# Kernel optimization log

Measured on AMD Instinct MI355X. Metric: run time of the kernel, lower is better.

The kernel has to match this reference:

```python
import jax, jax.numpy as jnp
import numpy as np

S, B, D1, D2 = 256, 128, 1024, 1024
H1 = (D1 + D1) // 2  # 1024
H2 = (D1 + D2) // 2  # 1024


def setup_inputs() -> dict:
    key = jax.random.key(0)
    ks = jax.random.split(key, 11)
    s = lambda k, shp, fan_in: jax.random.normal(k, shp, jnp.float32) * (1.0 / np.sqrt(fan_in))
    return {
        "feature1": jax.random.normal(ks[0], (B, D1), jnp.float32),
        "feature2": jax.random.normal(ks[1], (B, D2), jnp.float32),
        "feature1_seq": jax.random.normal(ks[2], (S, B, D1), jnp.float32),
        "W11": s(ks[3], (2 * D1, H1), 2 * D1),
        "b11": jnp.zeros((H1,), jnp.float32),
        "W12": s(ks[4], (D1 + D2, H2), D1 + D2),
        "b12": jnp.zeros((H2,), jnp.float32),
        "W21": s(ks[5], (H1, 1), H1),
        "b21": jnp.zeros((1,), jnp.float32),
        "W22": s(ks[6], (H2, 1), H2),
        "b22": jnp.zeros((1,), jnp.float32),
    }


def reference(feature1, feature2, feature1_seq, W11, b11, W12, b12, W21, b21, W22, b22):
    # feature1_seq: [S, B, D1]; feature1: [B, D1]; feature2: [B, D2]
    seq_len = feature1_seq.shape[0]
    f1 = jnp.broadcast_to(feature1[None], (seq_len,) + feature1.shape)  # [S,B,D1]
    f2 = jnp.broadcast_to(feature2[None], (seq_len,) + feature2.shape)  # [S,B,D2]
    h1 = jnp.tanh(jnp.concatenate([feature1_seq, f1], axis=-1) @ W11 + b11)  # [S,B,H1]
    h2 = jnp.tanh(jnp.concatenate([feature1_seq, f2], axis=-1) @ W12 + b12)  # [S,B,H2]
    s1 = h1 @ W21 + b21  # [S,B,1]
    s2 = h2 @ W22 + b22  # [S,B,1]
    w1 = jax.nn.softmax(s1, axis=0)  # softmax over sequence dim
    w2 = jax.nn.softmax(s2, axis=0)
    # mean over sequence of (w1+w2)*seq/2 -> [B, D1]
    return jnp.mean((w1 + w2) * feature1_seq * 0.5, axis=0)
```

## Files before the change

### kernel.cpp

```cpp
#include <hip/hip_runtime.h>

#define S_LEN 256
#define B_SZ  128
#define M_ROWS (S_LEN * B_SZ)

typedef __attribute__((ext_vector_type(8))) short bf16x8;
typedef __attribute__((ext_vector_type(4))) float f32x4;

__device__ __forceinline__ unsigned short f2bf(float x) {
    unsigned u = __float_as_uint(x);
    unsigned r = (u + 0x7fffu + ((u >> 16) & 1u)) >> 16;
    return (unsigned short)r;
}

__device__ __forceinline__ void gl_lds16(const void* g, void* l) {
    __builtin_amdgcn_global_load_lds(
        (const __attribute__((address_space(1))) unsigned int*)g,
        (__attribute__((address_space(3))) unsigned int*)l,
        16, 0, 0);
}

__global__ __launch_bounds__(256) void convert_seq(const float* __restrict__ in,
                                                   unsigned short* __restrict__ out,
                                                   long n4) {
    long i = (long)blockIdx.x * blockDim.x + threadIdx.x;
    long stride = (long)gridDim.x * blockDim.x;
    for (; i < n4; i += stride) {
        float4 v = ((const float4*)in)[i];
        ushort4 o;
        o.x = f2bf(v.x); o.y = f2bf(v.y); o.z = f2bf(v.z); o.w = f2bf(v.w);
        ((ushort4*)out)[i] = o;
    }
}

__global__ __launch_bounds__(256) void convert_f(const float* __restrict__ f1,
                                                 const float* __restrict__ f2,
                                                 unsigned short* __restrict__ out) {
    int g = blockIdx.x * 256 + threadIdx.x;
    float4 v = (g < 32768) ? ((const float4*)f1)[g] : ((const float4*)f2)[g - 32768];
    ushort4 o;
    o.x = f2bf(v.x); o.y = f2bf(v.y); o.z = f2bf(v.z); o.w = f2bf(v.w);
    ((ushort4*)out)[g] = o;
}

__global__ __launch_bounds__(256) void transpose_w(const float* __restrict__ W11,
                                                   const float* __restrict__ W12,
                                                   unsigned short* __restrict__ Wt) {
    const int nt = blockIdx.x, kt = blockIdx.y, layer = blockIdx.z;
    const float* W = layer ? W12 : W11;
    __shared__ float T[64][65];
    const int c = threadIdx.x & 63, r4 = threadIdx.x >> 6;
    const int k0 = kt * 64, n0 = nt * 64;
    #pragma unroll
    for (int p = 0; p < 16; ++p) {
        int r = p * 4 + r4;
        T[r][c] = W[(size_t)(k0 + r) * 1024 + n0 + c];
    }
    __syncthreads();
    unsigned short* Wl = Wt + (size_t)layer * 1024 * 2048;
    #pragma unroll
    for (int p = 0; p < 16; ++p) {
        int n = p * 4 + r4;
        Wl[(size_t)(n0 + n) * 2048 + k0 + c] = f2bf(T[c][n]);
    }
}

__global__ __launch_bounds__(256) void c_precompute(const unsigned short* __restrict__ fbf,
                                                    const unsigned short* __restrict__ Wt,
                                                    const float* __restrict__ b11,
                                                    const float* __restrict__ b12,
                                                    float* __restrict__ cbuf) {
    __shared__ char smem[32768];
    unsigned short* ldsA = (unsigned short*)smem;
    unsigned short* ldsB = (unsigned short*)(smem + 16384);
    const int n0 = blockIdx.x * 128;
    const int layer = blockIdx.y;
    const int tid = threadIdx.x;
    const int w = tid >> 6, l = tid & 63;
    const int wm = w >> 1, wn = w & 1;
    const int lr = l & 15, lg = l >> 4;
    const unsigned short* Af = fbf + (size_t)layer * 128 * 1024;
    const unsigned short* Wl = Wt + (size_t)layer * 1024 * 2048;
    const float* bias = layer ? b12 : b11;

    f32x4 acc[4][4];
    #pragma unroll
    for (int i = 0; i < 4; ++i)
        #pragma unroll
        for (int j = 0; j < 4; ++j)
            #pragma unroll
            for (int e = 0; e < 4; ++e) acc[i][j][e] = 0.f;

    for (int kk = 0; kk < 1024; kk += 64) {
        __syncthreads();
        #pragma unroll
        for (int c = 0; c < 4; ++c) {
            int o = w * 4096 + c * 1024;
            int ob = o + l * 16;
            int row = ob >> 7, kb = ob & 127;
            gl_lds16((const char*)Af + ((size_t)row * 1024 + kk) * 2 + kb, (char*)ldsA + o);
            gl_lds16((const char*)Wl + ((size_t)(n0 + row) * 2048 + 1024 + kk) * 2 + kb, (char*)ldsB + o);
        }
        __syncthreads();
        #pragma unroll
        for (int ks = 0; ks < 2; ++ks) {
            bf16x8 av[4], bv[4];
            #pragma unroll
            for (int i = 0; i < 4; ++i) {
                av[i] = *(const bf16x8*)(ldsA + (wm * 64 + i * 16 + lr) * 64 + ks * 32 + lg * 8);
                bv[i] = *(const bf16x8*)(ldsB + (wn * 64 + i * 16 + lr) * 64 + ks * 32 + lg * 8);
            }
            #pragma unroll
            for (int i = 0; i < 4; ++i)
                #pragma unroll
                for (int j = 0; j < 4; ++j)
                    acc[i][j] = __builtin_amdgcn_mfma_f32_16x16x32_bf16(av[i], bv[j], acc[i][j], 0, 0, 0);
        }
    }
    float* cl = cbuf + (size_t)layer * 128 * 1024;
    #pragma unroll
    for (int i = 0; i < 4; ++i)
        #pragma unroll
        for (int j = 0; j < 4; ++j)
            #pragma unroll
            for (int q = 0; q < 4; ++q) {
                int rr = wm * 64 + i * 16 + lg * 4 + q;
                int hc = n0 + wn * 64 + j * 16 + lr;
                cl[(size_t)rr * 1024 + hc] = acc[i][j][q] + bias[hc];
            }
}


__global__ __launch_bounds__(1024, 4) void fused_main(const unsigned short* __restrict__ Abf,
                                                      const unsigned short* __restrict__ Wt,
                                                      const float* __restrict__ cbuf,
                                                      const float* __restrict__ W21,
                                                      const float* __restrict__ W22,
                                                      float* __restrict__ sbufp) {
    __shared__ char smem[131072];
    const int bid = blockIdx.x;
    const int xcd = bid & 7;
    const int idx = bid >> 3;
    const int mtq = (idx & 3) + 4 * (idx >> 5);
    const int g   = (idx >> 2) & 7;
    const int mt  = xcd + 8 * mtq;
    const int layer = g >> 2;
    const int nt    = g & 3;
    const int n0 = nt * 256;

    const int tid = threadIdx.x;
    const int w = tid >> 6, l = tid & 63;
    const int wm = w >> 2, wn = w & 3;
    const int lr = l & 15, lg = l >> 4;

    const char* Ag = (const char*)Abf + (size_t)mt * 256 * 2048;
    const char* Bg = (const char*)(Wt + (size_t)layer * 1024 * 2048) + (size_t)n0 * 4096;

    const int dloc = tid * 16;
    const int gsw  = dloc ^ ((dloc >> 3) & 0x70);
    const char* srcA = Ag + (size_t)(gsw >> 7) * 2048 + (gsw & 127);
    const char* srcB = Bg + (size_t)(gsw >> 7) * 4096 + (gsw & 127);
    const int dstT = w * 1024;

    const int xr = (lr & 7) << 4;
    int offA[4], offB[4];
    #pragma unroll
    for (int i = 0; i < 4; ++i) {
        offA[i] = (wm * 64 + i * 16 + lr) * 128 + ((lg * 16) ^ xr);
        offB[i] = (wn * 64 + i * 16 + lr) * 128 + ((lg * 16) ^ xr);
    }

    f32x4 acc[4][4];
    #pragma unroll
    for (int i = 0; i < 4; ++i)
        #pragma unroll
        for (int j = 0; j < 4; ++j)
            #pragma unroll
            for (int e = 0; e < 4; ++e) acc[i][j][e] = 0.f;

#define STAGE(t, bi) do {                                               \
        char* d_ = smem + (bi) * 65536;                                 \
        const char* a_ = srcA + (size_t)(t) * 128;                      \
        const char* b_ = srcB + (size_t)(t) * 128;                      \
        gl_lds16(a_,              d_ +         dstT);                   \
        gl_lds16(a_ + 128 * 2048, d_ + 16384 + dstT);                   \
        gl_lds16(b_,              d_ + 32768 + dstT);                   \
        gl_lds16(b_ + 128 * 4096, d_ + 49152 + dstT);                   \
    } while (0)

#define COMPUTE(bi) do {                                                \
        const char* Ab_ = smem + (bi) * 65536;                          \
        const char* Bb_ = Ab_ + 32768;                                  \
        bf16x8 a0_[4], b0_[4], a1_[4], b1_[4];                          \
        _Pragma("unroll")                                               \
        for (int i_ = 0; i_ < 4; ++i_) {                                \
            a0_[i_] = *(const bf16x8*)(Ab_ + offA[i_]);                 \
            b0_[i_] = *(const bf16x8*)(Bb_ + offB[i_]);                 \
            a1_[i_] = *(const bf16x8*)(Ab_ + (offA[i_] ^ 64));          \
            b1_[i_] = *(const bf16x8*)(Bb_ + (offB[i_] ^ 64));          \
        }                                                               \
        _Pragma("unroll")                                               \
        for (int i_ = 0; i_ < 4; ++i_)                                  \
            _Pragma("unroll")                                           \
            for (int j_ = 0; j_ < 4; ++j_)                              \
                acc[i_][j_] = __builtin_amdgcn_mfma_f32_16x16x32_bf16(  \
                    a0_[i_], b0_[j_], acc[i_][j_], 0, 0, 0);            \
        _Pragma("unroll")                                               \
        for (int i_ = 0; i_ < 4; ++i_)                                  \
            _Pragma("unroll")                                           \
            for (int j_ = 0; j_ < 4; ++j_)                              \
                acc[i_][j_] = __builtin_amdgcn_mfma_f32_16x16x32_bf16(  \
                    a1_[i_], b1_[j_], acc[i_][j_], 0, 0, 0);            \
    } while (0)

    STAGE(0, 0);
    __builtin_amdgcn_sched_barrier(0);
    asm volatile("s_waitcnt vmcnt(0)" ::: "memory");
    __builtin_amdgcn_sched_barrier(0);
    __builtin_amdgcn_s_barrier();
    __builtin_amdgcn_sched_barrier(0);

    for (int t = 0; t < 16; ++t) {
        const int cur = t & 1;
        if (t < 15) STAGE(t + 1, cur ^ 1);
        COMPUTE(cur);
        __builtin_amdgcn_sched_barrier(0);
        asm volatile("s_waitcnt vmcnt(0)" ::: "memory");
        __builtin_amdgcn_sched_barrier(0);
        __builtin_amdgcn_s_barrier();
        __builtin_amdgcn_sched_barrier(0);
    }

#undef STAGE
#undef COMPUTE

    const float* cl = cbuf + (size_t)layer * 131072;
    const float* W2 = layer ? W22 : W21;
    float w2v[4];
    #pragma unroll
    for (int j = 0; j < 4; ++j) w2v[j] = W2[n0 + wn * 64 + j * 16 + lr];
    float* red = (float*)smem;
    #pragma unroll
    for (int i = 0; i < 4; ++i) {
        #pragma unroll
        for (int q = 0; q < 4; ++q) {
            int wrow = wm * 64 + i * 16 + lg * 4 + q;
            int brow = wrow & 127;
            float p = 0.f;
            #pragma unroll
            for (int j = 0; j < 4; ++j) {
                int col = n0 + wn * 64 + j * 16 + lr;
                float z = acc[i][j][q] + cl[(size_t)brow * 1024 + col];
                float e = __expf(2.f * z);
                p += (1.f - 2.f / (e + 1.f)) * w2v[j];
            }
            p += __shfl_xor(p, 1);
            p += __shfl_xor(p, 2);
            p += __shfl_xor(p, 4);
            p += __shfl_xor(p, 8);
            if (lr == 0) red[wrow * 4 + wn] = p;
        }
    }
    __syncthreads();
    if (tid < 256) {
        float v = red[tid * 4 + 0] + red[tid * 4 + 1] + red[tid * 4 + 2] + red[tid * 4 + 3];
        sbufp[(size_t)g * M_ROWS + (size_t)mt * 256 + tid] = v;
    }
}

__device__ __forceinline__ float block_max(float v, float* lds) {
    #pragma unroll
    for (int m = 32; m; m >>= 1) v = fmaxf(v, __shfl_xor(v, m));
    if ((threadIdx.x & 63) == 0) lds[threadIdx.x >> 6] = v;
    __syncthreads();
    v = fmaxf(fmaxf(lds[0], lds[1]), fmaxf(lds[2], lds[3]));
    __syncthreads();
    return v;
}
__device__ __forceinline__ float block_sum(float v, float* lds) {
    #pragma unroll
    for (int m = 32; m; m >>= 1) v += __shfl_xor(v, m);
    if ((threadIdx.x & 63) == 0) lds[threadIdx.x >> 6] = v;
    __syncthreads();
    v = lds[0] + lds[1] + lds[2] + lds[3];
    __syncthreads();
    return v;
}

__global__ __launch_bounds__(256) void coef_kernel(const float* __restrict__ sbufp,
                                                   float* __restrict__ coef) {
    __shared__ float lds[4];
    const int b = blockIdx.x, s = threadIdx.x;
    float v1 = 0.f, v2 = 0.f;
    #pragma unroll
    for (int nt = 0; nt < 4; ++nt) {
        v1 += sbufp[(size_t)nt * M_ROWS + (size_t)s * 128 + b];
        v2 += sbufp[(size_t)(4 + nt) * M_ROWS + (size_t)s * 128 + b];
    }
    float m1 = block_max(v1, lds);
    float e1 = expf(v1 - m1);
    float S1 = block_sum(e1, lds);
    float m2 = block_max(v2, lds);
    float e2 = expf(v2 - m2);
    float S2 = block_sum(e2, lds);
    coef[(size_t)s * 128 + b] = (e1 / S1 + e2 / S2) * (0.5f / (float)S_LEN);
}

__global__ __launch_bounds__(256) void final_kernel(const float* __restrict__ seq,
                                                    const float* __restrict__ coef,
                                                    float* __restrict__ out) {
    const int b = blockIdx.x, dq = blockIdx.y;
    const int d = dq * 256 + threadIdx.x;
    float a = 0.f;
    #pragma unroll 8
    for (int s = 0; s < 256; ++s) {
        a += coef[(size_t)s * 128 + b] * seq[(size_t)(s * 128 + b) * 1024 + d];
    }
    out[(size_t)b * 1024 + d] = a;
}

extern "C" void kernel_launch(void* const* d_in, const int* in_sizes, int n_in,
                              void* d_out, int out_size, void* d_ws, size_t ws_size,
                              hipStream_t stream) {
    const float* feature1 = (const float*)d_in[0];
    const float* feature2 = (const float*)d_in[1];
    const float* seq      = (const float*)d_in[2];
    const float* W11      = (const float*)d_in[3];
    const float* b11      = (const float*)d_in[4];
    const float* W12      = (const float*)d_in[5];
    const float* b12      = (const float*)d_in[6];
    const float* W21      = (const float*)d_in[7];
    const float* W22      = (const float*)d_in[9];
    float* out = (float*)d_out;

    char* ws = (char*)d_ws;
    unsigned short* Abf   = (unsigned short*)(ws + 0);
    unsigned short* Wt    = (unsigned short*)(ws + 67108864);
    unsigned short* fbf   = (unsigned short*)(ws + 75497472);
    float*          cbuf  = (float*)(ws + 76021760);
    float*          sbufp = (float*)(ws + 77070336);
    float*          coef  = (float*)(ws + 78118912);

    convert_seq<<<2048, 256, 0, stream>>>(seq, Abf, (long)M_ROWS * 1024 / 4);
    convert_f<<<256, 256, 0, stream>>>(feature1, feature2, fbf);
    transpose_w<<<dim3(16, 32, 2), 256, 0, stream>>>(W11, W12, Wt);
    c_precompute<<<dim3(8, 2), 256, 0, stream>>>(fbf, Wt, b11, b12, cbuf);
    fused_main<<<1024, 1024, 0, stream>>>(Abf, Wt, cbuf, W21, W22, sbufp);
    coef_kernel<<<128, 256, 0, stream>>>(sbufp, coef);
    final_kernel<<<dim3(128, 4), 256, 0, stream>>>(seq, coef, out);
}
```

Before: 231.8 us.

## Shrink fused GEMM tile to 128x256 with 512 threads and smaller K-step

The main fused GEMM+tanh+score kernel moves from 256x256 tiles with 1024 threads and 64-wide K steps to 128x256 tiles with 512 threads and 32-wide K steps. The grid doubles to 2048 blocks and LDS use drops from 128KB to 48KB per block, with a new swizzle for the 64-byte rows and a manually unrolled double-buffer loop. The aim is more resident blocks per CU and better latency hiding and load balance. The cost is lower B-tile reuse per block and twice as many barriers per unit of K.

```diff
diff --git a/kernel.cpp b/kernel.cpp
--- a/kernel.cpp
+++ b/kernel.cpp
@@ -131,19 +131,18 @@
 }
 
 
-__global__ __launch_bounds__(1024, 4) void fused_main(const unsigned short* __restrict__ Abf,
-                                                      const unsigned short* __restrict__ Wt,
-                                                      const float* __restrict__ cbuf,
-                                                      const float* __restrict__ W21,
-                                                      const float* __restrict__ W22,
-                                                      float* __restrict__ sbufp) {
-    __shared__ char smem[131072];
+__global__ __launch_bounds__(512, 4) void fused_main(const unsigned short* __restrict__ Abf,
+                                                     const unsigned short* __restrict__ Wt,
+                                                     const float* __restrict__ cbuf,
+                                                     const float* __restrict__ W21,
+                                                     const float* __restrict__ W22,
+                                                     float* __restrict__ sbufp) {
+    __shared__ char smem[49152];
     const int bid = blockIdx.x;
     const int xcd = bid & 7;
     const int idx = bid >> 3;
-    const int mtq = (idx & 3) + 4 * (idx >> 5);
-    const int g   = (idx >> 2) & 7;
-    const int mt  = xcd + 8 * mtq;
+    const int g   = idx & 7;
+    const int mt  = xcd + 8 * (idx >> 3);
     const int layer = g >> 2;
     const int nt    = g & 3;
     const int n0 = nt * 256;
@@ -153,21 +152,27 @@
     const int wm = w >> 2, wn = w & 3;
     const int lr = l & 15, lg = l >> 4;
 
-    const char* Ag = (const char*)Abf + (size_t)mt * 256 * 2048;
+    const char* Ag = (const char*)Abf + (size_t)mt * 128 * 2048;
     const char* Bg = (const char*)(Wt + (size_t)layer * 1024 * 2048) + (size_t)n0 * 4096;
 
-    const int dloc = tid * 16;
-    const int gsw  = dloc ^ ((dloc >> 3) & 0x70);
-    const char* srcA = Ag + (size_t)(gsw >> 7) * 2048 + (gsw & 127);
-    const char* srcB = Bg + (size_t)(gsw >> 7) * 4096 + (gsw & 127);
-    const int dstT = w * 1024;
-
-    const int xr = (lr & 7) << 4;
+    const int dlocA  = tid * 16;
+    const int gswA   = dlocA ^ (((dlocA >> 7) & 3) << 4);
+    const char* srcA = Ag + (size_t)(gswA >> 6) * 2048 + (gswA & 63);
+    const int dlocB0 = tid * 16;
+    const int gswB0  = dlocB0 ^ (((dlocB0 >> 7) & 3) << 4);
+    const char* srcB0 = Bg + (size_t)(gswB0 >> 6) * 4096 + (gswB0 & 63);
+    const int dlocB1 = 8192 + tid * 16;
+    const int gswB1  = dlocB1 ^ (((dlocB1 >> 7) & 3) << 4);
+    const char* srcB1 = Bg + (size_t)(gswB1 >> 6) * 4096 + (gswB1 & 63);
+    const int dstW = w * 1024;
+
     int offA[4], offB[4];
     #pragma unroll
     for (int i = 0; i < 4; ++i) {
-        offA[i] = (wm * 64 + i * 16 + lr) * 128 + ((lg * 16) ^ xr);
-        offB[i] = (wn * 64 + i * 16 + lr) * 128 + ((lg * 16) ^ xr);
+        int oa = (wm * 64 + i * 16 + lr) * 64 + lg * 16;
+        offA[i] = oa ^ (((oa >> 7) & 3) << 4);
+        int ob = (wn * 64 + i * 16 + lr) * 64 + lg * 16;
+        offB[i] = ob ^ (((ob >> 7) & 3) << 4);
     }
 
     f32x4 acc[4][4];
@@ -179,60 +184,50 @@
             for (int e = 0; e < 4; ++e) acc[i][j][e] = 0.f;
 
 #define STAGE(t, bi) do {                                               \
-        char* d_ = smem + (bi) * 65536;                                 \
-        const char* a_ = srcA + (size_t)(t) * 128;                      \
-        const char* b_ = srcB + (size_t)(t) * 128;                      \
-        gl_lds16(a_,              d_ +         dstT);                   \
-        gl_lds16(a_ + 128 * 2048, d_ + 16384 + dstT);                   \
-        gl_lds16(b_,              d_ + 32768 + dstT);                   \
-        gl_lds16(b_ + 128 * 4096, d_ + 49152 + dstT);                   \
+        char* d_ = smem + (bi) * 24576;                                 \
+        gl_lds16(srcA  + (size_t)(t) * 64, d_ + dstW);                  \
+        gl_lds16(srcB0 + (size_t)(t) * 64, d_ + 8192 + dstW);           \
+        gl_lds16(srcB1 + (size_t)(t) * 64, d_ + 16384 + dstW);          \
     } while (0)
 
 #define COMPUTE(bi) do {                                                \
-        const char* Ab_ = smem + (bi) * 65536;                          \
-        const char* Bb_ = Ab_ + 32768;                                  \
-        bf16x8 a0_[4], b0_[4], a1_[4], b1_[4];                          \
+        const char* Ab_ = smem + (bi) * 24576;                          \
+        const char* Bb_ = Ab_ + 8192;                                   \
+        bf16x8 av_[4], bv_[4];                                          \
         _Pragma("unroll")                                               \
         for (int i_ = 0; i_ < 4; ++i_) {                                \
-            a0_[i_] = *(const bf16x8*)(Ab_ + offA[i_]);                 \
-            b0_[i_] = *(const bf16x8*)(Bb_ + offB[i_]);                 \
-            a1_[i_] = *(const bf16x8*)(Ab_ + (offA[i_] ^ 64));          \
-            b1_[i_] = *(const bf16x8*)(Bb_ + (offB[i_] ^ 64));          \
+            av_[i_] = *(const bf16x8*)(Ab_ + offA[i_]);                 \
+            bv_[i_] = *(const bf16x8*)(Bb_ + offB[i_]);                 \
         }                                                               \
         _Pragma("unroll")                                               \
         for (int i_ = 0; i_ < 4; ++i_)                                  \
             _Pragma("unroll")                                           \
             for (int j_ = 0; j_ < 4; ++j_)                              \
                 acc[i_][j_] = __builtin_amdgcn_mfma_f32_16x16x32_bf16(  \
-                    a0_[i_], b0_[j_], acc[i_][j_], 0, 0, 0);            \
-        _Pragma("unroll")                                               \
-        for (int i_ = 0; i_ < 4; ++i_)                                  \
-            _Pragma("unroll")                                           \
-            for (int j_ = 0; j_ < 4; ++j_)                              \
-                acc[i_][j_] = __builtin_amdgcn_mfma_f32_16x16x32_bf16(  \
-                    a1_[i_], b1_[j_], acc[i_][j_], 0, 0, 0);            \
+                    av_[i_], bv_[j_], acc[i_][j_], 0, 0, 0);            \
     } while (0)
 
+#define WAITBAR() do {                                                  \
+        __builtin_amdgcn_sched_barrier(0);                              \
+        asm volatile("s_waitcnt vmcnt(0)" ::: "memory");                \
+        __builtin_amdgcn_sched_barrier(0);                              \
+        __builtin_amdgcn_s_barrier();                                   \
+        __builtin_amdgcn_sched_barrier(0);                              \
+    } while (0)
+
     STAGE(0, 0);
-    __builtin_amdgcn_sched_barrier(0);
-    asm volatile("s_waitcnt vmcnt(0)" ::: "memory");
-    __builtin_amdgcn_sched_barrier(0);
-    __builtin_amdgcn_s_barrier();
-    __builtin_amdgcn_sched_barrier(0);
-
-    for (int t = 0; t < 16; ++t) {
-        const int cur = t & 1;
-        if (t < 15) STAGE(t + 1, cur ^ 1);
-        COMPUTE(cur);
-        __builtin_amdgcn_sched_barrier(0);
-        asm volatile("s_waitcnt vmcnt(0)" ::: "memory");
-        __builtin_amdgcn_sched_barrier(0);
-        __builtin_amdgcn_s_barrier();
-        __builtin_amdgcn_sched_barrier(0);
+    WAITBAR();
+
+    for (int tt = 0; tt < 32; tt += 2) {
+        if (tt + 1 < 32) STAGE(tt + 1, 1);
+        COMPUTE(0); WAITBAR();
+        if (tt + 2 < 32) STAGE(tt + 2, 0);
+        COMPUTE(1); WAITBAR();
     }
 
 #undef STAGE
 #undef COMPUTE
+#undef WAITBAR
 
     const float* cl = cbuf + (size_t)layer * 131072;
     const float* W2 = layer ? W22 : W21;
@@ -245,12 +240,11 @@
         #pragma unroll
         for (int q = 0; q < 4; ++q) {
             int wrow = wm * 64 + i * 16 + lg * 4 + q;
-            int brow = wrow & 127;
             float p = 0.f;
             #pragma unroll
             for (int j = 0; j < 4; ++j) {
                 int col = n0 + wn * 64 + j * 16 + lr;
-                float z = acc[i][j][q] + cl[(size_t)brow * 1024 + col];
+                float z = acc[i][j][q] + cl[(size_t)wrow * 1024 + col];
                 float e = __expf(2.f * z);
                 p += (1.f - 2.f / (e + 1.f)) * w2v[j];
             }
@@ -262,9 +256,9 @@
         }
     }
     __syncthreads();
-    if (tid < 256) {
+    if (tid < 128) {
         float v = red[tid * 4 + 0] + red[tid * 4 + 1] + red[tid * 4 + 2] + red[tid * 4 + 3];
-        sbufp[(size_t)g * M_ROWS + (size_t)mt * 256 + tid] = v;
+        sbufp[(size_t)g * M_ROWS + (size_t)mt * 128 + tid] = v;
     }
 }
 
@@ -345,7 +339,7 @@
     convert_f<<<256, 256, 0, stream>>>(feature1, feature2, fbf);
     transpose_w<<<dim3(16, 32, 2), 256, 0, stream>>>(W11, W12, Wt);
     c_precompute<<<dim3(8, 2), 256, 0, stream>>>(fbf, Wt, b11, b12, cbuf);
-    fused_main<<<1024, 1024, 0, stream>>>(Abf, Wt, cbuf, W21, W22, sbufp);
+    fused_main<<<2048, 512, 0, stream>>>(Abf, Wt, cbuf, W21, W22, sbufp);
     coef_kernel<<<128, 256, 0, stream>>>(sbufp, coef);
     final_kernel<<<dim3(128, 4), 256, 0, stream>>>(seq, coef, out);
 }
```

New measurement: 249.8 us. 1.08x slower.

## Load A operand directly from global into registers, stage only B in LDS

Applied to the files above, without the earlier changes.

The A tile is no longer staged through shared memory. Each lane now loads its A fragments straight from global memory into registers, and only the B (weight) tile is double-buffered in LDS, which halves the shared memory footprint. This removes the LDS write/read traffic for A and could let more blocks fit per CU. In exchange, the direct global A loads are exposed within each k-step because the vmcnt(0) wait sits right after they are issued, and A is fetched per wave without reuse across wave columns, so it goes through L1/L2 repeatedly.

```diff
diff --git a/kernel.cpp b/kernel.cpp
--- a/kernel.cpp
+++ b/kernel.cpp
@@ -137,7 +137,7 @@
                                                       const float* __restrict__ W21,
                                                       const float* __restrict__ W22,
                                                       float* __restrict__ sbufp) {
-    __shared__ char smem[131072];
+    __shared__ char smem[65536];
     const int bid = blockIdx.x;
     const int xcd = bid & 7;
     const int idx = bid >> 3;
@@ -158,17 +158,16 @@
 
     const int dloc = tid * 16;
     const int gsw  = dloc ^ ((dloc >> 3) & 0x70);
-    const char* srcA = Ag + (size_t)(gsw >> 7) * 2048 + (gsw & 127);
     const char* srcB = Bg + (size_t)(gsw >> 7) * 4096 + (gsw & 127);
     const int dstT = w * 1024;
 
     const int xr = (lr & 7) << 4;
-    int offA[4], offB[4];
-    #pragma unroll
-    for (int i = 0; i < 4; ++i) {
-        offA[i] = (wm * 64 + i * 16 + lr) * 128 + ((lg * 16) ^ xr);
+    int offB[4];
+    #pragma unroll
+    for (int i = 0; i < 4; ++i)
         offB[i] = (wn * 64 + i * 16 + lr) * 128 + ((lg * 16) ^ xr);
-    }
+
+    const char* aLane = Ag + (size_t)(wm * 64 + lr) * 2048 + (size_t)(lg * 16);
 
     f32x4 acc[4][4];
     #pragma unroll
@@ -178,61 +177,57 @@
             #pragma unroll
             for (int e = 0; e < 4; ++e) acc[i][j][e] = 0.f;
 
-#define STAGE(t, bi) do {                                               \
-        char* d_ = smem + (bi) * 65536;                                 \
-        const char* a_ = srcA + (size_t)(t) * 128;                      \
-        const char* b_ = srcB + (size_t)(t) * 128;                      \
-        gl_lds16(a_,              d_ +         dstT);                   \
-        gl_lds16(a_ + 128 * 2048, d_ + 16384 + dstT);                   \
-        gl_lds16(b_,              d_ + 32768 + dstT);                   \
-        gl_lds16(b_ + 128 * 4096, d_ + 49152 + dstT);                   \
+#define STAGEB(t, bi) do {                                              \
+        char* d_ = smem + (bi) * 32768;                                 \
+        gl_lds16(srcB + (size_t)(t) * 128,              d_ +         dstT); \
+        gl_lds16(srcB + (size_t)(t) * 128 + 128 * 4096, d_ + 16384 + dstT); \
     } while (0)
 
-#define COMPUTE(bi) do {                                                \
-        const char* Ab_ = smem + (bi) * 65536;                          \
-        const char* Bb_ = Ab_ + 32768;                                  \
-        bf16x8 a0_[4], b0_[4], a1_[4], b1_[4];                          \
+#define KTILE(t, bi) do {                                               \
+        bf16x8 av_[8];                                                  \
         _Pragma("unroll")                                               \
         for (int i_ = 0; i_ < 4; ++i_) {                                \
-            a0_[i_] = *(const bf16x8*)(Ab_ + offA[i_]);                 \
-            b0_[i_] = *(const bf16x8*)(Bb_ + offB[i_]);                 \
-            a1_[i_] = *(const bf16x8*)(Ab_ + (offA[i_] ^ 64));          \
-            b1_[i_] = *(const bf16x8*)(Bb_ + (offB[i_] ^ 64));          \
+            const char* ap_ = aLane + i_ * 32768 + (size_t)(t) * 128;   \
+            av_[i_ * 2 + 0] = *(const bf16x8*)(ap_);                    \
+            av_[i_ * 2 + 1] = *(const bf16x8*)(ap_ + 64);               \
         }                                                               \
+        __builtin_amdgcn_sched_barrier(0);   \
+        if ((t) < 15) STAGEB((t) + 1, (bi) ^ 1);                        \
+        const char* Bb_ = smem + (bi) * 32768;                          \
         _Pragma("unroll")                                               \
-        for (int i_ = 0; i_ < 4; ++i_)                                  \
+        for (int ks_ = 0; ks_ < 2; ++ks_) {                             \
+            bf16x8 bv_[4];                                              \
             _Pragma("unroll")                                           \
             for (int j_ = 0; j_ < 4; ++j_)                              \
-                acc[i_][j_] = __builtin_amdgcn_mfma_f32_16x16x32_bf16(  \
-                    a0_[i_], b0_[j_], acc[i_][j_], 0, 0, 0);            \
-        _Pragma("unroll")                                               \
-        for (int i_ = 0; i_ < 4; ++i_)                                  \
+                bv_[j_] = *(const bf16x8*)(Bb_ + (offB[j_] ^ (ks_ * 64))); \
             _Pragma("unroll")                                           \
-            for (int j_ = 0; j_ < 4; ++j_)                              \
-                acc[i_][j_] = __builtin_amdgcn_mfma_f32_16x16x32_bf16(  \
-                    a1_[i_], b1_[j_], acc[i_][j_], 0, 0, 0);            \
+            for (int i_ = 0; i_ < 4; ++i_)                              \
+                _Pragma("unroll")                                       \
+                for (int j_ = 0; j_ < 4; ++j_)                          \
+                    acc[i_][j_] = __builtin_amdgcn_mfma_f32_16x16x32_bf16( \
+                        av_[i_ * 2 + ks_], bv_[j_], acc[i_][j_], 0, 0, 0); \
+        }                                                               \
     } while (0)
 
-    STAGE(0, 0);
-    __builtin_amdgcn_sched_barrier(0);
-    asm volatile("s_waitcnt vmcnt(0)" ::: "memory");
-    __builtin_amdgcn_sched_barrier(0);
-    __builtin_amdgcn_s_barrier();
-    __builtin_amdgcn_sched_barrier(0);
-
-    for (int t = 0; t < 16; ++t) {
-        const int cur = t & 1;
-        if (t < 15) STAGE(t + 1, cur ^ 1);
-        COMPUTE(cur);
-        __builtin_amdgcn_sched_barrier(0);
-        asm volatile("s_waitcnt vmcnt(0)" ::: "memory");
-        __builtin_amdgcn_sched_barrier(0);
-        __builtin_amdgcn_s_barrier();
-        __builtin_amdgcn_sched_barrier(0);
-    }
-
-#undef STAGE
-#undef COMPUTE
+#define WAITBAR() do {                                                  \
+        __builtin_amdgcn_sched_barrier(0);                              \
+        asm volatile("s_waitcnt vmcnt(0)" ::: "memory");                \
+        __builtin_amdgcn_sched_barrier(0);                              \
+        __builtin_amdgcn_s_barrier();                                   \
+        __builtin_amdgcn_sched_barrier(0);                              \
+    } while (0)
+
+    STAGEB(0, 0);
+    WAITBAR();
+
+    for (int tt = 0; tt < 16; tt += 2) {
+        KTILE(tt, 0);     WAITBAR();
+        KTILE(tt + 1, 1); WAITBAR();
+    }
+
+#undef STAGEB
+#undef KTILE
+#undef WAITBAR
 
     const float* cl = cbuf + (size_t)layer * 131072;
     const float* W2 = layer ? W22 : W21;
```

After: 500.4 us. 116% more time.

## Triple-buffer A tiles and prefetch two steps ahead in fused GEMM

Applied to the files above, without the earlier changes.

Splits the LDS staging into separate A and B buffers. A tiles are now triple-buffered and fetched two K-steps ahead, while B stays double-buffered one step ahead. Waits use vmcnt(2) instead of draining all loads, so more global-to-LDS traffic overlaps with MFMA compute. LDS per block grows from 128KB to 160KB, and the loop is fully unrolled with explicit buffer indices.

```diff
diff --git a/kernel.cpp b/kernel.cpp
--- a/kernel.cpp
+++ b/kernel.cpp
@@ -137,7 +137,7 @@
                                                       const float* __restrict__ W21,
                                                       const float* __restrict__ W22,
                                                       float* __restrict__ sbufp) {
-    __shared__ char smem[131072];
+    __shared__ char smem[163840];
     const int bid = blockIdx.x;
     const int xcd = bid & 7;
     const int idx = bid >> 3;
@@ -178,19 +178,23 @@
             #pragma unroll
             for (int e = 0; e < 4; ++e) acc[i][j][e] = 0.f;
 
-#define STAGE(t, bi) do {                                               \
-        char* d_ = smem + (bi) * 65536;                                 \
+#define STAGE_A(t, ta) do {                                             \
+        char* d_ = smem + (ta) * 32768;                                 \
         const char* a_ = srcA + (size_t)(t) * 128;                      \
+        gl_lds16(a_,          d_ +         dstT);                       \
+        gl_lds16(a_ + 262144, d_ + 16384 + dstT);                       \
+    } while (0)
+
+#define STAGE_B(t, tb) do {                                             \
+        char* d_ = smem + 98304 + (tb) * 32768;                         \
         const char* b_ = srcB + (size_t)(t) * 128;                      \
-        gl_lds16(a_,              d_ +         dstT);                   \
-        gl_lds16(a_ + 128 * 2048, d_ + 16384 + dstT);                   \
-        gl_lds16(b_,              d_ + 32768 + dstT);                   \
-        gl_lds16(b_ + 128 * 4096, d_ + 49152 + dstT);                   \
-    } while (0)
-
-#define COMPUTE(bi) do {                                                \
-        const char* Ab_ = smem + (bi) * 65536;                          \
-        const char* Bb_ = Ab_ + 32768;                                  \
+        gl_lds16(b_,          d_ +         dstT);                       \
+        gl_lds16(b_ + 524288, d_ + 16384 + dstT);                       \
+    } while (0)
+
+#define COMPUTE(ta, tb) do {                                            \
+        const char* Ab_ = smem + (ta) * 32768;                          \
+        const char* Bb_ = smem + 98304 + (tb) * 32768;                  \
         bf16x8 a0_[4], b0_[4], a1_[4], b1_[4];                          \
         _Pragma("unroll")                                               \
         for (int i_ = 0; i_ < 4; ++i_) {                                \
@@ -213,26 +217,51 @@
                     a1_[i_], b1_[j_], acc[i_][j_], 0, 0, 0);            \
     } while (0)
 
-    STAGE(0, 0);
-    __builtin_amdgcn_sched_barrier(0);
-    asm volatile("s_waitcnt vmcnt(0)" ::: "memory");
-    __builtin_amdgcn_sched_barrier(0);
-    __builtin_amdgcn_s_barrier();
-    __builtin_amdgcn_sched_barrier(0);
-
-    for (int t = 0; t < 16; ++t) {
-        const int cur = t & 1;
-        if (t < 15) STAGE(t + 1, cur ^ 1);
-        COMPUTE(cur);
-        __builtin_amdgcn_sched_barrier(0);
-        asm volatile("s_waitcnt vmcnt(0)" ::: "memory");
-        __builtin_amdgcn_sched_barrier(0);
-        __builtin_amdgcn_s_barrier();
-        __builtin_amdgcn_sched_barrier(0);
-    }
-
-#undef STAGE
+#define WAITBAR(n) do {                                                 \
+        __builtin_amdgcn_sched_barrier(0);                              \
+        asm volatile("s_waitcnt vmcnt(" #n ")" ::: "memory");           \
+        __builtin_amdgcn_sched_barrier(0);                              \
+        __builtin_amdgcn_s_barrier();                                   \
+        __builtin_amdgcn_sched_barrier(0);                              \
+    } while (0)
+
+    STAGE_B(0, 0);
+    STAGE_A(0, 0);
+    STAGE_A(1, 1);
+    WAITBAR(2);
+
+#define ITER(t, ta, tb, tb1, ta2) do {                                  \
+        STAGE_B((t) + 1, tb1);                                          \
+        STAGE_A((t) + 2, ta2);                                          \
+        COMPUTE(ta, tb);                                                \
+        WAITBAR(2);                                                     \
+    } while (0)
+
+    ITER(0, 0, 0, 1, 2);
+    ITER(1, 1, 1, 0, 0);
+    ITER(2, 2, 0, 1, 1);
+    ITER(3, 0, 1, 0, 2);
+    ITER(4, 1, 0, 1, 0);
+    ITER(5, 2, 1, 0, 1);
+    ITER(6, 0, 0, 1, 2);
+    ITER(7, 1, 1, 0, 0);
+    ITER(8, 2, 0, 1, 1);
+    ITER(9, 0, 1, 0, 2);
+    ITER(10, 1, 0, 1, 0);
+    ITER(11, 2, 1, 0, 1);
+    ITER(12, 0, 0, 1, 2);
+    ITER(13, 1, 1, 0, 0);
+    STAGE_B(15, 1);
+    COMPUTE(2, 0);
+    WAITBAR(0);
+    COMPUTE(0, 1);
+    WAITBAR(0);
+
+#undef ITER
+#undef STAGE_A
+#undef STAGE_B
 #undef COMPUTE
+#undef WAITBAR
 
     const float* cl = cbuf + (size_t)layer * 131072;
     const float* W2 = layer ? W22 : W21;
```

New measurement: 251.8 us. +8.6%, slower.
